# Kernel optimization log

Hardware: AMD Instinct MI355X
Metric: run time of the kernel (lower is better)

Reference implementation:

```python
import jax, jax.numpy as jnp
import numpy as np

MAXV = 8  # convex quad clipped by convex quad has at most 8 vertices


def _cr(u, v):
    return u[..., 0] * v[..., 1] - u[..., 1] * v[..., 0]


def quad_intersection_area(subj, clip):
    """Area of intersection of two convex quads via Sutherland-Hodgman.
    subj, clip: [4,2]. Replaces the pyclipper CT_INTERSECTION + Area() call."""
    # orient clip polygon CCW so the half-plane inside test (cross >= 0) is correct
    x, y = clip[:, 0], clip[:, 1]
    sa = jnp.sum(x * jnp.roll(y, -1) - jnp.roll(x, -1) * y)
    clip = jnp.where(sa < 0, clip[::-1], clip)
    edges = jnp.stack([clip, jnp.roll(clip, -1, axis=0)], axis=1)  # [4,2,2]

    pts0 = jnp.zeros((MAXV, 2), subj.dtype).at[:4].set(subj)
    n0 = jnp.int32(4)

    def clip_step(carry, edge):
        pts, n = carry
        a, b = edge[0], edge[1]
        idx = jnp.arange(MAXV)
        valid = idx < n
        nxt = jnp.where(idx + 1 >= n, 0, idx + 1)
        p, q = pts, pts[nxt]
        dp = _cr(b - a, p - a)
        dq = _cr(b - a, q - a)
        in_p, in_q = dp >= 0, dq >= 0
        denom = dp - dq
        t = jnp.where(denom == 0, 0.0, dp / jnp.where(denom == 0, 1.0, denom))
        ip = p + t[:, None] * (q - p)
        out_pts = jnp.stack([p, ip], axis=1).reshape(2 * MAXV, 2)
        out_valid = jnp.stack([valid & in_p, valid & (in_p != in_q)], axis=1).reshape(2 * MAXV)
        order = jnp.argsort(~out_valid)  # stable: valid points compacted to front
        new_pts = out_pts[order][:MAXV]
        new_n = jnp.minimum(jnp.sum(out_valid), MAXV).astype(jnp.int32)
        return (new_pts, new_n), None

    (pts, n), _ = jax.lax.scan(clip_step, (pts0, n0), edges)
    idx = jnp.arange(MAXV)
    valid = idx < n
    nxt = jnp.where(idx + 1 >= n, 0, idx + 1)
    area = 0.5 * jnp.sum(jnp.where(valid, _cr(pts, pts[nxt]), 0.0))
    return jnp.abs(area)


def _degenerate(poly):
    # original skips any quad with two identical vertices
    pairs = [(0, 1), (0, 2), (0, 3), (1, 2), (1, 3), (2, 3)]
    return jnp.any(jnp.stack([jnp.all(poly[i] == poly[j]) for i, j in pairs]))


def _per_pic(boxes, scores, polys, labels, num_class):
    P = boxes.shape[0]
    subj = boxes[:, :8].reshape(P, 4, 2)
    area_fn = jax.vmap(jax.vmap(quad_intersection_area, in_axes=(0, None)),
                       in_axes=(None, 0))
    areas = area_fn(subj, polys)                      # [G, P]
    pred_deg = jax.vmap(_degenerate)(subj)            # [P]
    gt_deg = jax.vmap(_degenerate)(polys)             # [G]
    areas = jnp.where(pred_deg[None, :], 0.0, areas)
    gmax = jnp.argmax(areas, axis=1)                  # [G]
    best = jnp.take_along_axis(areas, gmax[:, None], 1)[:, 0]
    matched = (~gt_deg) & (best != 0)
    midx = jnp.where(matched, gmax, 0)
    # unmatched rows are zeroed, exactly like pred_class_score[indices]=0
    pred_scores = jnp.where(matched[:, None], scores[midx], 0.0)
    logp = jax.nn.log_softmax(pred_scores, axis=-1)
    onehot = jax.nn.one_hot(labels, num_class, dtype=logp.dtype)
    ce = -jnp.mean(jnp.sum(onehot * logp, axis=-1))   # CrossEntropyLoss w/ soft targets
    pred_num = jnp.where(matched, jnp.argmax(scores, axis=1)[midx], -1)
    correct = jnp.sum(pred_num == labels)
    return ce, correct


def _make_quads(key, shape_prefix, img=800.0):
    k1, k2, k3 = jax.random.split(key, 3)
    c = jax.random.uniform(k1, shape_prefix + (1, 2), minval=0.0, maxval=img)
    wh = jax.random.uniform(k2, shape_prefix + (1, 2), minval=4.0, maxval=24.0)
    base = jnp.array([[-1.0, -1.0], [1.0, -1.0], [1.0, 1.0], [-1.0, 1.0]])
    jit = jax.random.uniform(k3, shape_prefix + (4, 2), minval=-1.0, maxval=1.0)
    return c + base * wh + jit


def setup_inputs() -> dict:
    key = jax.random.key(0)
    B, P, G, C = 8, 512, 128, 68
    k1, k2, k3, k4, k5 = jax.random.split(key, 5)
    pred_quads = _make_quads(k1, (B, P))              # [B,P,4,2]
    box_score = jax.random.uniform(k2, (B, P, 1))
    char_bboxes = jnp.concatenate([pred_quads.reshape(B, P, 8), box_score], axis=-1)
    char_scores = jax.random.normal(k3, (B, P, C), dtype=jnp.float32)
    polygon_chars = _make_quads(k4, (B, G))           # [B,G,4,2]
    line_chars = jax.random.randint(k5, (B, G), 0, C, dtype=jnp.int32)
    return {"char_bboxes": char_bboxes, "char_scores": char_scores,
            "polygon_chars": polygon_chars, "line_chars": line_chars}


def reference(char_bboxes, char_scores, polygon_chars, line_chars):
    C = char_scores.shape[-1]
    ce, correct = jax.vmap(lambda b, s, p, l: _per_pic(b, s, p, l, C))(
        char_bboxes, char_scores, polygon_chars, line_chars)
    loss = jnp.mean(ce)
    total_number = jnp.int32(line_chars.shape[0] * line_chars.shape[1])
    rec_correct = jnp.sum(correct).astype(jnp.int32)
    return loss, total_number, rec_correct
```

## Files before the change

kernel.cpp:

```cpp
#include <hip/hip_runtime.h>
#include <math.h>

#define B_ 8
#define P_ 512
#define G_ 128
#define C_ 68
#define BG (B_ * G_)
#define BP (B_ * P_)
#define EPS_ 1.0f

#define CLIP_EDGE(E, INX, INY, OUTX, OUTY)                                   \
    {                                                                        \
        const float eax = ccx[E], eay = ccy[E];                              \
        const float ex = ccx[(E + 1) & 3] - eax;                             \
        const float ey = ccy[(E + 1) & 3] - eay;                             \
        float vx[8], vy[8], dp[8];                                           \
        bool  vin[8];                                                        \
        _Pragma("unroll")                                                    \
        for (int i = 0; i < 8; ++i) {                                        \
            vx[i] = INX[i * 64 + t];                                         \
            vy[i] = INY[i * 64 + t];                                         \
        }                                                                    \
        _Pragma("unroll")                                                    \
        for (int i = 0; i < 8; ++i) {                                        \
            dp[i]  = ex * (vy[i] - eay) - ey * (vx[i] - eax);                \
            vin[i] = (dp[i] >= 0.0f);                                        \
        }                                                                    \
        int m = 0;                                                           \
        _Pragma("unroll")                                                    \
        for (int i = 0; i < 8; ++i) {                                        \
            if (i < n) {                                                     \
                const bool wrap = (i + 1 == n);                              \
                const int  jn   = (i + 1) & 7;                               \
                const float qx = wrap ? vx[0] : vx[jn];                      \
                const float qy = wrap ? vy[0] : vy[jn];                      \
                const float dq = wrap ? dp[0] : dp[jn];                      \
                const bool  inq = (dq >= 0.0f);                              \
                if (vin[i]) {                                                \
                    if (m < 8) { OUTX[m * 64 + t] = vx[i];                   \
                                 OUTY[m * 64 + t] = vy[i]; }                 \
                    ++m;                                                     \
                }                                                            \
                if (vin[i] != inq) {                                         \
                    const float den = dp[i] - dq;                            \
                    const float tt = (den == 0.0f) ? 0.0f : dp[i] / den;     \
                    if (m < 8) {                                             \
                        OUTX[m * 64 + t] = vx[i] + tt * (qx - vx[i]);        \
                        OUTY[m * 64 + t] = vy[i] + tt * (qy - vy[i]);        \
                    }                                                        \
                    ++m;                                                     \
                }                                                            \
            }                                                                \
        }                                                                    \
        n = (m > 8) ? 8 : m;                                                 \
    }

__global__ __launch_bounds__(64) void match_kernel(
    const float* __restrict__ bboxes,
    const float* __restrict__ scores,
    const float* __restrict__ polys,
    const int*   __restrict__ labels,
    float* __restrict__ ce_out,
    int*   __restrict__ corr_out)
{
#pragma clang fp contract(off)
    const int bg = blockIdx.x;
    const int b  = bg >> 7;
    const int t  = threadIdx.x;

    __shared__ int   s_idx[P_];
    __shared__ float s_px[8 * 64], s_py[8 * 64];
    __shared__ float s_qx[8 * 64], s_qy[8 * 64];

    const float* cp = polys + (size_t)bg * 8;
    const float x0 = cp[0], y0 = cp[1], x1 = cp[2], y1 = cp[3];
    const float x2 = cp[4], y2 = cp[5], x3 = cp[6], y3 = cp[7];
    const float sa = (x0 * y1 - x1 * y0) + (x1 * y2 - x2 * y1)
                   + (x2 * y3 - x3 * y2) + (x3 * y0 - x0 * y3);
    const bool rev = (sa < 0.0f);
    float ccx[4], ccy[4];
    ccx[0] = rev ? x3 : x0; ccy[0] = rev ? y3 : y0;
    ccx[1] = rev ? x2 : x1; ccy[1] = rev ? y2 : y1;
    ccx[2] = rev ? x1 : x2; ccy[2] = rev ? y1 : y2;
    ccx[3] = rev ? x0 : x3; ccy[3] = rev ? y0 : y3;
    const bool gt_deg =
        (x0 == x1 && y0 == y1) || (x0 == x2 && y0 == y2) ||
        (x0 == x3 && y0 == y3) || (x1 == x2 && y1 == y2) ||
        (x1 == x3 && y1 == y3) || (x2 == x3 && y2 == y3);
    const float glox = fminf(fminf(x0, x1), fminf(x2, x3)) - EPS_;
    const float gloy = fminf(fminf(y0, y1), fminf(y2, y3)) - EPS_;
    const float ghix = fmaxf(fmaxf(x0, x1), fmaxf(x2, x3)) + EPS_;
    const float ghiy = fmaxf(fmaxf(y0, y1), fmaxf(y2, y3)) + EPS_;

    const float* bbb = bboxes + (size_t)b * P_ * 9;
    int base = 0;
    #pragma unroll
    for (int r = 0; r < 8; ++r) {
        const int p = t + (r << 6);
        const float* bb = bbb + (size_t)p * 9;
        const float a0 = bb[0], a1 = bb[1], a2 = bb[2], a3 = bb[3];
        const float a4 = bb[4], a5 = bb[5], a6 = bb[6], a7 = bb[7];
        const bool deg =
            (a0 == a2 && a1 == a3) || (a0 == a4 && a1 == a5) ||
            (a0 == a6 && a1 == a7) || (a2 == a4 && a3 == a5) ||
            (a2 == a6 && a3 == a7) || (a4 == a6 && a5 == a7);
        const float lox = fminf(fminf(a0, a2), fminf(a4, a6));
        const float loy = fminf(fminf(a1, a3), fminf(a5, a7));
        const float hix = fmaxf(fmaxf(a0, a2), fmaxf(a4, a6));
        const float hiy = fmaxf(fmaxf(a1, a3), fmaxf(a5, a7));
        const bool ov = !deg &&
            (lox <= ghix) && (glox <= hix) &&
            (loy <= ghiy) && (gloy <= hiy);
        const unsigned long long mask = __ballot(ov);
        if (ov) {
            const int pre = __builtin_amdgcn_mbcnt_hi(
                (unsigned int)(mask >> 32),
                __builtin_amdgcn_mbcnt_lo((unsigned int)mask, 0u));
            s_idx[base + pre] = p;
        }
        base += __popcll(mask);
    }
    const int ns = base;

    float bestA = 0.0f;
    int   bestI = 0x7fffffff;

    for (int k0 = 0; k0 < ns; k0 += 64) {
        const int k = k0 + t;
        if (k < ns) {
            const int p = s_idx[k];
            const float* bb = bbb + (size_t)p * 9;
            int n = 4;

            {
                float vx[4], vy[4], dp[4];
                bool  vin[4];
                vx[0] = bb[0]; vy[0] = bb[1];
                vx[1] = bb[2]; vy[1] = bb[3];
                vx[2] = bb[4]; vy[2] = bb[5];
                vx[3] = bb[6]; vy[3] = bb[7];
                const float eax = ccx[0], eay = ccy[0];
                const float ex = ccx[1] - eax;
                const float ey = ccy[1] - eay;
                #pragma unroll
                for (int i = 0; i < 4; ++i) {
                    dp[i]  = ex * (vy[i] - eay) - ey * (vx[i] - eax);
                    vin[i] = (dp[i] >= 0.0f);
                }
                int m = 0;
                #pragma unroll
                for (int i = 0; i < 4; ++i) {
                    const int j = (i + 1) & 3;
                    if (vin[i]) {
                        if (m < 8) { s_qx[m * 64 + t] = vx[i];
                                     s_qy[m * 64 + t] = vy[i]; }
                        ++m;
                    }
                    if (vin[i] != vin[j]) {
                        const float den = dp[i] - dp[j];
                        const float tt = (den == 0.0f) ? 0.0f : dp[i] / den;
                        if (m < 8) {
                            s_qx[m * 64 + t] = vx[i] + tt * (vx[j] - vx[i]);
                            s_qy[m * 64 + t] = vy[i] + tt * (vy[j] - vy[i]);
                        }
                        ++m;
                    }
                }
                n = (m > 8) ? 8 : m;
            }

            CLIP_EDGE(1, s_qx, s_qy, s_px, s_py)
            CLIP_EDGE(2, s_px, s_py, s_qx, s_qy)
            CLIP_EDGE(3, s_qx, s_qy, s_px, s_py)

            float s = 0.0f;
            {
                float vx[8], vy[8];
                #pragma unroll
                for (int i = 0; i < 8; ++i) {
                    vx[i] = s_px[i * 64 + t];
                    vy[i] = s_py[i * 64 + t];
                }
                #pragma unroll
                for (int i = 0; i < 8; ++i) {
                    if (i < n) {
                        const bool wrap = (i + 1 == n);
                        const int  jn   = (i + 1) & 7;
                        const float qx = wrap ? vx[0] : vx[jn];
                        const float qy = wrap ? vy[0] : vy[jn];
                        s += vx[i] * qy - qx * vy[i];
                    }
                }
            }
            const float area = fabsf(0.5f * s);
            if (area > bestA || (area == bestA && p < bestI)) {
                bestA = area; bestI = p;
            }
        }
    }

    #pragma unroll
    for (int off = 32; off; off >>= 1) {
        const float oa = __shfl_xor(bestA, off);
        const int   oi = __shfl_xor(bestI, off);
        if (oa > bestA || (oa == bestA && oi < bestI)) { bestA = oa; bestI = oi; }
    }

    const bool matched = (!gt_deg) && (bestA != 0.0f);
    const int label = labels[bg];

    if (matched) {
        const float* sc = scores + (size_t)(b * P_ + bestI) * C_;
        const float v0 = sc[t];
        const bool  h2 = (t + 64) < C_;
        const float v1 = h2 ? sc[t + 64] : -3e38f;
        float bv; int bi;
        if (v1 > v0) { bv = v1; bi = t + 64; } else { bv = v0; bi = t; }
        float mx = fmaxf(v0, v1);
        #pragma unroll
        for (int off = 32; off; off >>= 1) mx = fmaxf(mx, __shfl_xor(mx, off));
        #pragma unroll
        for (int off = 32; off; off >>= 1) {
            const float ov2 = __shfl_xor(bv, off);
            const int   oi2 = __shfl_xor(bi, off);
            if (ov2 > bv || (ov2 == bv && oi2 < bi)) { bv = ov2; bi = oi2; }
        }
        float e = expf(v0 - mx) + (h2 ? expf(v1 - mx) : 0.0f);
        #pragma unroll
        for (int off = 32; off; off >>= 1) e += __shfl_xor(e, off);
        if (t == 0) {
            ce_out[bg]   = mx + logf(e) - sc[label];
            corr_out[bg] = (bi == label) ? 1 : 0;
        }
    } else {
        if (t == 0) {
            ce_out[bg]   = logf((float)C_);
            corr_out[bg] = 0;
        }
    }
}

__global__ __launch_bounds__(256) void finalize_kernel(
    const float* __restrict__ ce,
    const int*   __restrict__ corr,
    float* __restrict__ out)
{
    const int t = threadIdx.x;
    float a = ce[t] + ce[t + 256] + ce[t + 512] + ce[t + 768];
    int   c = corr[t] + corr[t + 256] + corr[t + 512] + corr[t + 768];
    #pragma unroll
    for (int off = 32; off; off >>= 1) {
        a += __shfl_xor(a, off);
        c += __shfl_xor(c, off);
    }
    __shared__ float pa[4];
    __shared__ int   pc[4];
    if ((t & 63) == 0) { pa[t >> 6] = a; pc[t >> 6] = c; }
    __syncthreads();
    if (t == 0) {
        const float s = (pa[0] + pa[1]) + (pa[2] + pa[3]);
        const int  cc = (pc[0] + pc[1]) + (pc[2] + pc[3]);
        out[0] = s / (float)BG;
        out[1] = (float)BG;
        out[2] = (float)cc;
    }
}

extern "C" void kernel_launch(void* const* d_in, const int* in_sizes, int n_in,
                              void* d_out, int out_size, void* d_ws, size_t ws_size,
                              hipStream_t stream) {
    const float* bboxes = (const float*)d_in[0];
    const float* scores = (const float*)d_in[1];
    const float* polys  = (const float*)d_in[2];
    const int*   labels = (const int*)d_in[3];
    float* out = (float*)d_out;

    float* ce = (float*)d_ws;
    int*   cr = (int*)((char*)d_ws + BG * sizeof(float));

    match_kernel<<<BG, 64, 0, stream>>>(bboxes, scores, polys, labels, ce, cr);
    finalize_kernel<<<1, 256, 0, stream>>>(ce, cr, out);
}
```

Baseline: 16.59 us.

## Split bbox overlap prefilter across four wavefronts per block

The block grows from one wavefront to four. Each wavefront prefilters 128 of the 512 predicted boxes against the ground-truth box bounds and writes its survivors into its own segment. After a barrier, wavefront 0 alone does the polygon clipping, finding each candidate index through segment offsets. This shortens the serial 8-round prefilter loop, at the cost of a __syncthreads, three idle wavefronts, and more per-candidate indexing work.

```diff
diff --git a/kernel.cpp b/kernel.cpp
--- a/kernel.cpp
+++ b/kernel.cpp
@@ -18,8 +18,8 @@
         bool  vin[8];                                                        \
         _Pragma("unroll")                                                    \
         for (int i = 0; i < 8; ++i) {                                        \
-            vx[i] = INX[i * 64 + t];                                         \
-            vy[i] = INY[i * 64 + t];                                         \
+            vx[i] = INX[i * 64 + lane];                                      \
+            vy[i] = INY[i * 64 + lane];                                      \
         }                                                                    \
         _Pragma("unroll")                                                    \
         for (int i = 0; i < 8; ++i) {                                        \
@@ -37,16 +37,16 @@
                 const float dq = wrap ? dp[0] : dp[jn];                      \
                 const bool  inq = (dq >= 0.0f);                              \
                 if (vin[i]) {                                                \
-                    if (m < 8) { OUTX[m * 64 + t] = vx[i];                   \
-                                 OUTY[m * 64 + t] = vy[i]; }                 \
+                    if (m < 8) { OUTX[m * 64 + lane] = vx[i];                \
+                                 OUTY[m * 64 + lane] = vy[i]; }              \
                     ++m;                                                     \
                 }                                                            \
                 if (vin[i] != inq) {                                         \
                     const float den = dp[i] - dq;                            \
                     const float tt = (den == 0.0f) ? 0.0f : dp[i] / den;     \
                     if (m < 8) {                                             \
-                        OUTX[m * 64 + t] = vx[i] + tt * (qx - vx[i]);        \
-                        OUTY[m * 64 + t] = vy[i] + tt * (qy - vy[i]);        \
+                        OUTX[m * 64 + lane] = vx[i] + tt * (qx - vx[i]);     \
+                        OUTY[m * 64 + lane] = vy[i] + tt * (qy - vy[i]);     \
                     }                                                        \
                     ++m;                                                     \
                 }                                                            \
@@ -55,7 +55,7 @@
         n = (m > 8) ? 8 : m;                                                 \
     }
 
-__global__ __launch_bounds__(64) void match_kernel(
+__global__ __launch_bounds__(256) void match_kernel(
     const float* __restrict__ bboxes,
     const float* __restrict__ scores,
     const float* __restrict__ polys,
@@ -64,11 +64,14 @@
     int*   __restrict__ corr_out)
 {
 #pragma clang fp contract(off)
-    const int bg = blockIdx.x;
-    const int b  = bg >> 7;
-    const int t  = threadIdx.x;
-
-    __shared__ int   s_idx[P_];
+    const int bg   = blockIdx.x;
+    const int b    = bg >> 7;
+    const int t    = threadIdx.x;
+    const int w    = t >> 6;
+    const int lane = t & 63;
+
+    __shared__ int   s_seg[4 * 128];
+    __shared__ int   s_cnt[4];
     __shared__ float s_px[8 * 64], s_py[8 * 64];
     __shared__ float s_qx[8 * 64], s_qy[8 * 64];
 
@@ -93,42 +96,53 @@
     const float ghiy = fmaxf(fmaxf(y0, y1), fmaxf(y2, y3)) + EPS_;
 
     const float* bbb = bboxes + (size_t)b * P_ * 9;
-    int base = 0;
-    #pragma unroll
-    for (int r = 0; r < 8; ++r) {
-        const int p = t + (r << 6);
-        const float* bb = bbb + (size_t)p * 9;
-        const float a0 = bb[0], a1 = bb[1], a2 = bb[2], a3 = bb[3];
-        const float a4 = bb[4], a5 = bb[5], a6 = bb[6], a7 = bb[7];
-        const bool deg =
-            (a0 == a2 && a1 == a3) || (a0 == a4 && a1 == a5) ||
-            (a0 == a6 && a1 == a7) || (a2 == a4 && a3 == a5) ||
-            (a2 == a6 && a3 == a7) || (a4 == a6 && a5 == a7);
-        const float lox = fminf(fminf(a0, a2), fminf(a4, a6));
-        const float loy = fminf(fminf(a1, a3), fminf(a5, a7));
-        const float hix = fmaxf(fmaxf(a0, a2), fmaxf(a4, a6));
-        const float hiy = fmaxf(fmaxf(a1, a3), fmaxf(a5, a7));
-        const bool ov = !deg &&
-            (lox <= ghix) && (glox <= hix) &&
-            (loy <= ghiy) && (gloy <= hiy);
-        const unsigned long long mask = __ballot(ov);
-        if (ov) {
-            const int pre = __builtin_amdgcn_mbcnt_hi(
-                (unsigned int)(mask >> 32),
-                __builtin_amdgcn_mbcnt_lo((unsigned int)mask, 0u));
-            s_idx[base + pre] = p;
-        }
-        base += __popcll(mask);
-    }
-    const int ns = base;
+    {
+        int base = 0;
+        #pragma unroll
+        for (int r = 0; r < 2; ++r) {
+            const int p = (w << 7) + (r << 6) + lane;
+            const float* bb = bbb + (size_t)p * 9;
+            const float a0 = bb[0], a1 = bb[1], a2 = bb[2], a3 = bb[3];
+            const float a4 = bb[4], a5 = bb[5], a6 = bb[6], a7 = bb[7];
+            const bool deg =
+                (a0 == a2 && a1 == a3) || (a0 == a4 && a1 == a5) ||
+                (a0 == a6 && a1 == a7) || (a2 == a4 && a3 == a5) ||
+                (a2 == a6 && a3 == a7) || (a4 == a6 && a5 == a7);
+            const float lox = fminf(fminf(a0, a2), fminf(a4, a6));
+            const float loy = fminf(fminf(a1, a3), fminf(a5, a7));
+            const float hix = fmaxf(fmaxf(a0, a2), fmaxf(a4, a6));
+            const float hiy = fmaxf(fmaxf(a1, a3), fmaxf(a5, a7));
+            const bool ov = !deg &&
+                (lox <= ghix) && (glox <= hix) &&
+                (loy <= ghiy) && (gloy <= hiy);
+            const unsigned long long mask = __ballot(ov);
+            if (ov) {
+                const int pre = __builtin_amdgcn_mbcnt_hi(
+                    (unsigned int)(mask >> 32),
+                    __builtin_amdgcn_mbcnt_lo((unsigned int)mask, 0u));
+                s_seg[(w << 7) + base + pre] = p;
+            }
+            base += __popcll(mask);
+        }
+        if (lane == 0) s_cnt[w] = base;
+    }
+    __syncthreads();
+
+    if (w != 0) return;
+
+    const int c0 = s_cnt[0], c1 = s_cnt[1], c2 = s_cnt[2], c3 = s_cnt[3];
+    const int o1 = c0, o2 = c0 + c1, o3 = c0 + c1 + c2;
+    const int ns = o3 + c3;
 
     float bestA = 0.0f;
     int   bestI = 0x7fffffff;
 
     for (int k0 = 0; k0 < ns; k0 += 64) {
-        const int k = k0 + t;
+        const int k = k0 + lane;
         if (k < ns) {
-            const int p = s_idx[k];
+            const int ws  = (k >= o1 ? 1 : 0) + (k >= o2 ? 1 : 0) + (k >= o3 ? 1 : 0);
+            const int off = (k >= o3) ? o3 : ((k >= o2) ? o2 : ((k >= o1) ? o1 : 0));
+            const int p   = s_seg[(ws << 7) + (k - off)];
             const float* bb = bbb + (size_t)p * 9;
             int n = 4;
 
@@ -152,16 +166,16 @@
                 for (int i = 0; i < 4; ++i) {
                     const int j = (i + 1) & 3;
                     if (vin[i]) {
-                        if (m < 8) { s_qx[m * 64 + t] = vx[i];
-                                     s_qy[m * 64 + t] = vy[i]; }
+                        if (m < 8) { s_qx[m * 64 + lane] = vx[i];
+                                     s_qy[m * 64 + lane] = vy[i]; }
                         ++m;
                     }
                     if (vin[i] != vin[j]) {
                         const float den = dp[i] - dp[j];
                         const float tt = (den == 0.0f) ? 0.0f : dp[i] / den;
                         if (m < 8) {
-                            s_qx[m * 64 + t] = vx[i] + tt * (vx[j] - vx[i]);
-                            s_qy[m * 64 + t] = vy[i] + tt * (vy[j] - vy[i]);
+                            s_qx[m * 64 + lane] = vx[i] + tt * (vx[j] - vx[i]);
+                            s_qy[m * 64 + lane] = vy[i] + tt * (vy[j] - vy[i]);
                         }
                         ++m;
                     }
@@ -178,8 +192,8 @@
                 float vx[8], vy[8];
                 #pragma unroll
                 for (int i = 0; i < 8; ++i) {
-                    vx[i] = s_px[i * 64 + t];
-                    vy[i] = s_py[i * 64 + t];
+                    vx[i] = s_px[i * 64 + lane];
+                    vy[i] = s_py[i * 64 + lane];
                 }
                 #pragma unroll
                 for (int i = 0; i < 8; ++i) {
@@ -211,11 +225,11 @@
 
     if (matched) {
         const float* sc = scores + (size_t)(b * P_ + bestI) * C_;
-        const float v0 = sc[t];
-        const bool  h2 = (t + 64) < C_;
-        const float v1 = h2 ? sc[t + 64] : -3e38f;
+        const float v0 = sc[lane];
+        const bool  h2 = (lane + 64) < C_;
+        const float v1 = h2 ? sc[lane + 64] : -3e38f;
         float bv; int bi;
-        if (v1 > v0) { bv = v1; bi = t + 64; } else { bv = v0; bi = t; }
+        if (v1 > v0) { bv = v1; bi = lane + 64; } else { bv = v0; bi = lane; }
         float mx = fmaxf(v0, v1);
         #pragma unroll
         for (int off = 32; off; off >>= 1) mx = fmaxf(mx, __shfl_xor(mx, off));
@@ -228,12 +242,12 @@
         float e = expf(v0 - mx) + (h2 ? expf(v1 - mx) : 0.0f);
         #pragma unroll
         for (int off = 32; off; off >>= 1) e += __shfl_xor(e, off);
-        if (t == 0) {
+        if (lane == 0) {
             ce_out[bg]   = mx + logf(e) - sc[label];
             corr_out[bg] = (bi == label) ? 1 : 0;
         }
     } else {
-        if (t == 0) {
+        if (lane == 0) {
             ce_out[bg]   = logf((float)C_);
             corr_out[bg] = 0;
         }
@@ -278,6 +292,6 @@
     float* ce = (float*)d_ws;
     int*   cr = (int*)((char*)d_ws + BG * sizeof(float));
 
-    match_kernel<<<BG, 64, 0, stream>>>(bboxes, scores, polys, labels, ce, cr);
+    match_kernel<<<BG, 256, 0, stream>>>(bboxes, scores, polys, labels, ce, cr);
     finalize_kernel<<<1, 256, 0, stream>>>(ce, cr, out);
 }
```

New measurement: 15.00 us. -9.5%, faster.
